# Kernel optimization log

Measured on AMD Instinct MI355X. Metric: run time of the kernel, lower is better.

## Reference

```python
import jax, jax.numpy as jnp
import numpy as np

BS, NA, NE, NAL = 128, 16, 16, 15
OWN, ALD, END = 30, 10, 10
H, HD, HYP, NACT = 64, 4, 64, 22
OUT_E = ((END + 1) * H + 1) * HD  # hyper_enemy output dim (weights + unused bias part)
OUT_A = ALD * H * HD


def setup_inputs() -> dict:
    key = jax.random.key(0)
    ks = jax.random.split(key, 30)
    s = 0.05
    r = lambda i, shape: jax.random.normal(ks[i], shape, dtype=jnp.float32) * s
    return {
        'bs': BS,
        'own_feats': r(0, (BS * NA, OWN)),
        'ally_feats': r(1, (BS * NA * NAL, ALD)),
        'enemy_feats': r(2, (BS * NA * NE, END)),
        'hidden_state': r(3, (BS * NA, H)),
        'fc1_w': r(4, (OWN, H)), 'fc1_b': r(5, (H,)),
        'he_w1': r(6, (END, HYP)), 'he_b1': r(7, (HYP,)),
        'he_w2': r(8, (HYP, OUT_E)), 'he_b2': r(9, (OUT_E,)),
        'ha_w1': r(10, (ALD, HYP)), 'ha_b1': r(11, (HYP,)),
        'ha_w2': r(12, (HYP, OUT_A)), 'ha_b2': r(13, (OUT_A,)),
        'merger_w': jnp.ones((1, HD, H), dtype=jnp.float32),
        'gru_wih': r(14, (3 * H, H)), 'gru_whh': r(15, (3 * H, H)),
        'gru_bih': r(16, (3 * H,)), 'gru_bhh': r(17, (3 * H,)),
        'fc2_w1': r(18, (H, H)), 'fc2_b1': r(19, (H,)),
        'fc2_w2': r(20, (H, NACT - 3)), 'fc2_b2': r(21, (NACT - 3,)),
        'pass_w1': r(22, (H, H)), 'pass_b1': r(23, (H,)),
        'pass_w2': r(24, (H, 3)), 'pass_b2': r(25, (3,)),
    }


def reference(bs, own_feats, ally_feats, enemy_feats, hidden_state,
              fc1_w, fc1_b, he_w1, he_b1, he_w2, he_b2,
              ha_w1, ha_b1, ha_w2, ha_b2, merger_w,
              gru_wih, gru_whh, gru_bih, gru_bhh,
              fc2_w1, fc2_b1, fc2_w2, fc2_b2,
              pass_w1, pass_b1, pass_w2, pass_b2):
    # own embedding: [bs*NA, H]
    emb_own = own_feats @ fc1_w + fc1_b

    # hypernet-generated enemy weights, consumed once then summed over enemies
    he = jax.nn.relu(enemy_feats @ he_w1 + he_b1) @ he_w2 + he_b2  # [bs*NA*NE, OUT_E]
    w_en = he[:, :END * H * HD].reshape(-1, END, H * HD)
    emb_en = jnp.einsum('ri,rio->ro', enemy_feats, w_en)
    emb_en = emb_en.reshape(bs * NA, NE, HD, H).sum(axis=1)  # [bs*NA, HD, H]

    ha = jax.nn.relu(ally_feats @ ha_w1 + ha_b1) @ ha_w2 + ha_b2  # [bs*NA*NAL, OUT_A]
    w_al = ha.reshape(-1, ALD, H * HD)
    emb_al4 = jnp.einsum('ri,rio->ro', ally_feats, w_al).reshape(bs * NA, NAL, HD, H)

    # passing_mlp -> [bs*NA, NAL, HD, 3]; permute/mean over heads, max over allies
    p = jax.nn.relu(emb_al4 @ pass_w1 + pass_b1) @ pass_w2 + pass_b2
    passing_dim = jnp.transpose(p, (0, 1, 3, 2)).mean(axis=-1)  # [bs*NA, NAL, 3]
    passing_embed = passing_dim.max(axis=1)  # [bs*NA, 3]

    emb_al = emb_al4.sum(axis=1)  # [bs*NA, HD, H]

    # Merger over heads
    mw = jax.nn.softmax(merger_w, axis=1)  # [1, HD, H]
    merged = jnp.sum(mw * (emb_en + emb_al), axis=1)  # [bs*NA, H]

    x = jax.nn.relu(emb_own + merged)

    # GRUCell (torch gate order: r, z, n)
    h_in = hidden_state.reshape(-1, H)
    gi = x @ gru_wih.T + gru_bih
    gh = h_in @ gru_whh.T + gru_bhh
    ir, iz, inn = jnp.split(gi, 3, axis=-1)
    hr, hz, hn = jnp.split(gh, 3, axis=-1)
    rg = jax.nn.sigmoid(ir + hr)
    zg = jax.nn.sigmoid(iz + hz)
    ng = jnp.tanh(inn + rg * hn)
    hh = (1.0 - zg) * ng + zg * h_in

    q_normal = (jax.nn.relu(hh @ fc2_w1 + fc2_b1) @ fc2_w2 + fc2_b2).reshape(bs, NA, -1)
    pe = passing_embed.reshape(bs, NA, 3)
    q = jnp.concatenate([q_normal[:, :, :9], pe, q_normal[:, :, 9:]], axis=-1)
    return q.reshape(bs, NA, -1), hh.reshape(bs, NA, -1)
```

## Files before the change

kernel.cpp:

```cpp
#include <hip/hip_runtime.h>
#include <hip/hip_bf16.h>

#define RAG   2048
#define AROWS 30720
#define KP    672
#define QOFF  45056

typedef __attribute__((ext_vector_type(8))) short short8;
typedef __attribute__((ext_vector_type(4))) float f32x4;

__device__ inline unsigned short f2bf(float f){
    unsigned u = __float_as_uint(f);
    u += 0x7fffu + ((u >> 16) & 1u);
    return (unsigned short)(u >> 16);
}
__device__ inline float bf2f(unsigned short s){ return __uint_as_float(((unsigned)s) << 16); }
__device__ inline unsigned pack2(float a, float b){
    return (unsigned)f2bf(a) | ((unsigned)f2bf(b) << 16);
}

__global__ void __launch_bounds__(256) k_prep(
    const float* __restrict__ hew2, const float* __restrict__ heb2,
    const float* __restrict__ haw2, const float* __restrict__ hab2,
    const float* __restrict__ allyf, const float* __restrict__ haw1, const float* __restrict__ hab1,
    unsigned short* __restrict__ Bte, unsigned short* __restrict__ Bta,
    unsigned short* __restrict__ ha1)
{
    int bb = blockIdx.x, tid = threadIdx.x;
    if (bb < 256){
        int n = bb;
        for (int k = tid; k < KP; k += 256){
            unsigned short ve = 0, va = 0;
            if (k < 640){
                int h = k & 63, i = k >> 6;
                ve = f2bf(hew2[h*2820 + i*256 + n]);
                va = f2bf(haw2[h*2560 + i*256 + n]);
            } else if (k < 650){
                int i = k - 640;
                ve = f2bf(heb2[i*256 + n]);
                va = f2bf(hab2[i*256 + n]);
            }
            Bte[n*KP + k] = ve;
            Bta[n*KP + k] = va;
        }
    } else {
        int r = (bb - 256)*4 + (tid >> 6), h = tid & 63;
        const float* a = allyf + r*10;
        float s = hab1[h];
#pragma unroll
        for (int i = 0; i < 10; ++i) s = fmaf(a[i], haw1[i*64 + h], s);
        ha1[r*64 + h] = f2bf(fmaxf(s, 0.f));
    }
}

__global__ void __launch_bounds__(256) k_usum(
    const float* __restrict__ ef, const float* __restrict__ hew1, const float* __restrict__ heb1,
    const float* __restrict__ af, const unsigned short* __restrict__ ha1,
    unsigned short* __restrict__ usum)
{
    __shared__ float s_ef[16][10], s_af[15][10];
    __shared__ float s_he[16][64], s_ha[15][64];
    int ag = blockIdx.x, tid = threadIdx.x;
    if (tid < 160) s_ef[tid/10][tid%10] = ef[ag*160 + tid];
    if (tid < 150) s_af[tid/10][tid%10] = af[ag*150 + tid];
    __syncthreads();
    for (int idx = tid; idx < 16*64; idx += 256){
        int en = idx >> 6, h = idx & 63;
        float s = heb1[h];
#pragma unroll
        for (int i = 0; i < 10; ++i) s = fmaf(s_ef[en][i], hew1[i*64 + h], s);
        s_he[en][h] = fmaxf(s, 0.f);
    }
    for (int idx = tid; idx < 15*64; idx += 256){
        int l = idx >> 6, h = idx & 63;
        s_ha[l][h] = bf2f(ha1[(ag*15 + l)*64 + h]);
    }
    __syncthreads();
    for (int k = tid; k < KP; k += 256){
        float ue = 0.f, ua = 0.f;
        if (k < 640){
            int i = k >> 6, h = k & 63;
#pragma unroll
            for (int en = 0; en < 16; ++en) ue = fmaf(s_he[en][h], s_ef[en][i], ue);
#pragma unroll
            for (int l = 0; l < 15; ++l) ua = fmaf(s_ha[l][h], s_af[l][i], ua);
        } else if (k < 650){
            int i = k - 640;
#pragma unroll
            for (int en = 0; en < 16; ++en) ue += s_ef[en][i];
#pragma unroll
            for (int l = 0; l < 15; ++l) ua += s_af[l][i];
        }
        usum[ag*KP + k]         = f2bf(ue);
        usum[(RAG + ag)*KP + k] = f2bf(ua);
    }
}

__global__ void __launch_bounds__(256, 2) k_gemm(
    const unsigned short* __restrict__ Bte, const unsigned short* __restrict__ Bta,
    const unsigned short* __restrict__ ha1, const float* __restrict__ af,
    const unsigned short* __restrict__ usum,
    const float* __restrict__ pw1, const float* __restrict__ pb1,
    const float* __restrict__ pw2, const float* __restrict__ pb2,
    float* __restrict__ emb, float* __restrict__ p2)
{
    __shared__ __align__(16) char smem[46080];
    unsigned short* sB  = (unsigned short*)smem;
    unsigned short* sA  = (unsigned short*)(smem + 20480);
    unsigned short* sH  = (unsigned short*)(smem + 25600);
    unsigned short* sW1 = (unsigned short*)(smem + 36864);

    int tid = threadIdx.x;
    int w = tid >> 6;
    int lane = tid & 63;
    int l15 = lane & 15, quad = lane >> 4;
    int bb = blockIdx.x;

    f32x4 acc[4][4];
#pragma unroll
    for (int a = 0; a < 4; ++a)
#pragma unroll
    for (int b = 0; b < 4; ++b) acc[a][b] = (f32x4){0.f, 0.f, 0.f, 0.f};

    if (bb < 480){
        int row0 = bb * 64;
        int r = tid >> 2, c = tid & 3;
#pragma unroll
        for (int p = 0; p < 2; ++p){
            int ch = tid + p*256;
            int rr = ch >> 3, cc = ch & 7;
            *(uint4*)&sH[rr*72 + cc*8] = *(const uint4*)&ha1[(row0 + rr)*64 + cc*8];
        }
#pragma unroll
        for (int p = 0; p < 16; ++p){
            int idx = tid + p*256;
            sW1[(idx & 63)*72 + (idx >> 6)] = f2bf(pw1[idx]);
        }
        float af_reg[10];
        {
            const float* ap = af + (row0 + r)*10;
#pragma unroll
            for (int i = 0; i < 10; ++i) af_reg[i] = ap[i];
        }
        __syncthreads();
        float h1f[16];
        {
            uint4 ra = *(const uint4*)&sH[r*72 + c*8];
            uint4 rb = *(const uint4*)&sH[r*72 + 32 + c*8];
            unsigned va[4] = {ra.x, ra.y, ra.z, ra.w};
            unsigned vb[4] = {rb.x, rb.y, rb.z, rb.w};
#pragma unroll
            for (int q = 0; q < 4; ++q){
                h1f[q*2+0]   = __uint_as_float(va[q] << 16);
                h1f[q*2+1]   = __uint_as_float(va[q] & 0xffff0000u);
                h1f[8+q*2+0] = __uint_as_float(vb[q] << 16);
                h1f[8+q*2+1] = __uint_as_float(vb[q] & 0xffff0000u);
            }
        }
        const unsigned short* Btb = Bta + tid*KP;
#pragma unroll
        for (int i = 0; i < 10; ++i){
#pragma unroll
            for (int hb = 0; hb < 2; ++hb){
                int kt = i*64 + hb*32;
                __syncthreads();
                uint4 bq0 = *(const uint4*)&Btb[kt + 0];
                uint4 bq1 = *(const uint4*)&Btb[kt + 8];
                uint4 bq2 = *(const uint4*)&Btb[kt + 16];
                uint4 bq3 = *(const uint4*)&Btb[kt + 24];
                float avf = af_reg[i];
                uint4 pk;
                pk.x = pack2(h1f[hb*8+0]*avf, h1f[hb*8+1]*avf);
                pk.y = pack2(h1f[hb*8+2]*avf, h1f[hb*8+3]*avf);
                pk.z = pack2(h1f[hb*8+4]*avf, h1f[hb*8+5]*avf);
                pk.w = pack2(h1f[hb*8+6]*avf, h1f[hb*8+7]*avf);
                *(uint4*)&sA[r*40 + c*8] = pk;
                *(uint4*)&sB[tid*40 + 0]  = bq0;
                *(uint4*)&sB[tid*40 + 8]  = bq1;
                *(uint4*)&sB[tid*40 + 16] = bq2;
                *(uint4*)&sB[tid*40 + 24] = bq3;
                __syncthreads();
                short8 a_[4], b_[4];
#pragma unroll
                for (int mt = 0; mt < 4; ++mt) a_[mt] = *(const short8*)&sA[(mt*16 + l15)*40 + quad*8];
#pragma unroll
                for (int nt = 0; nt < 4; ++nt) b_[nt] = *(const short8*)&sB[(w*64 + nt*16 + l15)*40 + quad*8];
#pragma unroll
                for (int mt = 0; mt < 4; ++mt)
#pragma unroll
                for (int nt = 0; nt < 4; ++nt)
                    acc[mt][nt] = __builtin_amdgcn_mfma_f32_16x16x32_bf16(a_[mt], b_[nt], acc[mt][nt], 0, 0, 0);
            }
        }
        {
            int kt = 640;
            __syncthreads();
            uint4 bq0 = *(const uint4*)&Btb[kt + 0];
            uint4 bq1 = *(const uint4*)&Btb[kt + 8];
            uint4 bq2 = *(const uint4*)&Btb[kt + 16];
            uint4 bq3 = *(const uint4*)&Btb[kt + 24];
            float v0=0.f,v1=0.f,v2=0.f,v3=0.f,v4=0.f,v5=0.f,v6=0.f,v7=0.f;
            if (c == 0){ v0=af_reg[0]; v1=af_reg[1]; v2=af_reg[2]; v3=af_reg[3];
                         v4=af_reg[4]; v5=af_reg[5]; v6=af_reg[6]; v7=af_reg[7]; }
            else if (c == 1){ v0 = af_reg[8]; v1 = af_reg[9]; }
            uint4 pk;
            pk.x = pack2(v0, v1); pk.y = pack2(v2, v3);
            pk.z = pack2(v4, v5); pk.w = pack2(v6, v7);
            *(uint4*)&sA[r*40 + c*8] = pk;
            *(uint4*)&sB[tid*40 + 0]  = bq0;
            *(uint4*)&sB[tid*40 + 8]  = bq1;
            *(uint4*)&sB[tid*40 + 16] = bq2;
            *(uint4*)&sB[tid*40 + 24] = bq3;
            __syncthreads();
            short8 a_[4], b_[4];
#pragma unroll
            for (int mt = 0; mt < 4; ++mt) a_[mt] = *(const short8*)&sA[(mt*16 + l15)*40 + quad*8];
#pragma unroll
            for (int nt = 0; nt < 4; ++nt) b_[nt] = *(const short8*)&sB[(w*64 + nt*16 + l15)*40 + quad*8];
#pragma unroll
            for (int mt = 0; mt < 4; ++mt)
#pragma unroll
            for (int nt = 0; nt < 4; ++nt)
                acc[mt][nt] = __builtin_amdgcn_mfma_f32_16x16x32_bf16(a_[mt], b_[nt], acc[mt][nt], 0, 0, 0);
        }
        __syncthreads();
        unsigned short* sE = (unsigned short*)(smem + w*9216);
#pragma unroll
        for (int mt = 0; mt < 4; ++mt)
#pragma unroll
        for (int nt = 0; nt < 4; ++nt)
#pragma unroll
        for (int rg = 0; rg < 4; ++rg)
            sE[(mt*16 + quad*4 + rg)*72 + nt*16 + l15] = f2bf(acc[mt][nt][rg]);
        __syncthreads();
        f32x4 yacc[4][4];
#pragma unroll
        for (int a = 0; a < 4; ++a)
#pragma unroll
        for (int b = 0; b < 4; ++b) yacc[a][b] = (f32x4){0.f, 0.f, 0.f, 0.f};
#pragma unroll
        for (int kb = 0; kb < 2; ++kb){
            short8 ea[4], wb[4];
#pragma unroll
            for (int mt = 0; mt < 4; ++mt) ea[mt] = *(const short8*)&sE[(mt*16 + l15)*72 + kb*32 + quad*8];
#pragma unroll
            for (int ot = 0; ot < 4; ++ot) wb[ot] = *(const short8*)&sW1[(ot*16 + l15)*72 + kb*32 + quad*8];
#pragma unroll
            for (int mt = 0; mt < 4; ++mt)
#pragma unroll
            for (int ot = 0; ot < 4; ++ot)
                yacc[mt][ot] = __builtin_amdgcn_mfma_f32_16x16x32_bf16(ea[mt], wb[ot], yacc[mt][ot], 0, 0, 0);
        }
        float pb1v[4], w2r[4][3];
#pragma unroll
        for (int ot = 0; ot < 4; ++ot){
            pb1v[ot] = pb1[ot*16 + l15];
#pragma unroll
            for (int j = 0; j < 3; ++j) w2r[ot][j] = pw2[(ot*16 + l15)*3 + j];
        }
#pragma unroll
        for (int mt = 0; mt < 4; ++mt){
            float part[4][3];
#pragma unroll
            for (int rg = 0; rg < 4; ++rg)
#pragma unroll
            for (int j = 0; j < 3; ++j) part[rg][j] = 0.f;
#pragma unroll
            for (int ot = 0; ot < 4; ++ot)
#pragma unroll
            for (int rg = 0; rg < 4; ++rg){
                float yv = fmaxf(yacc[mt][ot][rg] + pb1v[ot], 0.f);
#pragma unroll
                for (int j = 0; j < 3; ++j) part[rg][j] = fmaf(yv, w2r[ot][j], part[rg][j]);
            }
#pragma unroll
            for (int off = 1; off < 16; off <<= 1)
#pragma unroll
            for (int rg = 0; rg < 4; ++rg)
#pragma unroll
            for (int j = 0; j < 3; ++j) part[rg][j] += __shfl_xor(part[rg][j], off, 64);
            if (l15 == 0){
#pragma unroll
                for (int rg = 0; rg < 4; ++rg)
#pragma unroll
                for (int j = 0; j < 3; ++j)
                    p2[(row0 + mt*16 + quad*4 + rg)*12 + w*3 + j] = part[rg][j] + pb2[j];
            }
        }
    } else {
        int row0 = (bb - 480) * 64;
        const unsigned short* Btb = ((row0 < RAG) ? Bte : Bta) + tid*KP;
        const unsigned short* Ab  = usum + (row0 + (tid >> 2))*KP + (tid & 3)*8;
        int r = tid >> 2, c = tid & 3;
        for (int kt = 0; kt < KP; kt += 32){
            __syncthreads();
            uint4 aq  = *(const uint4*)&Ab[kt];
            uint4 bq0 = *(const uint4*)&Btb[kt + 0];
            uint4 bq1 = *(const uint4*)&Btb[kt + 8];
            uint4 bq2 = *(const uint4*)&Btb[kt + 16];
            uint4 bq3 = *(const uint4*)&Btb[kt + 24];
            *(uint4*)&sA[r*40 + c*8] = aq;
            *(uint4*)&sB[tid*40 + 0]  = bq0;
            *(uint4*)&sB[tid*40 + 8]  = bq1;
            *(uint4*)&sB[tid*40 + 16] = bq2;
            *(uint4*)&sB[tid*40 + 24] = bq3;
            __syncthreads();
            short8 a_[4], b_[4];
#pragma unroll
            for (int mt = 0; mt < 4; ++mt) a_[mt] = *(const short8*)&sA[(mt*16 + l15)*40 + quad*8];
#pragma unroll
            for (int nt = 0; nt < 4; ++nt) b_[nt] = *(const short8*)&sB[(w*64 + nt*16 + l15)*40 + quad*8];
#pragma unroll
            for (int mt = 0; mt < 4; ++mt)
#pragma unroll
            for (int nt = 0; nt < 4; ++nt)
                acc[mt][nt] = __builtin_amdgcn_mfma_f32_16x16x32_bf16(a_[mt], b_[nt], acc[mt][nt], 0, 0, 0);
        }
#pragma unroll
        for (int mt = 0; mt < 4; ++mt)
#pragma unroll
        for (int nt = 0; nt < 4; ++nt)
#pragma unroll
        for (int rg = 0; rg < 4; ++rg)
            emb[(row0 + mt*16 + quad*4 + rg)*256 + w*64 + nt*16 + l15] = acc[mt][nt][rg];
    }
}

__global__ void __launch_bounds__(512) k_final(
    const float* __restrict__ own, const float* __restrict__ hidden,
    const float* __restrict__ fc1w, const float* __restrict__ fc1b,
    const float* __restrict__ mergw,
    const float* __restrict__ wih, const float* __restrict__ whh,
    const float* __restrict__ bih, const float* __restrict__ bhh,
    const float* __restrict__ f2w1, const float* __restrict__ f2b1,
    const float* __restrict__ f2w2, const float* __restrict__ f2b2,
    const float* __restrict__ emb, const float* __restrict__ p2,
    float* __restrict__ out)
{
    int tid = threadIdx.x;
    int al = tid >> 6, h = tid & 63;
    int ag = blockIdx.x * 8 + al;
    __shared__ float sx[8][64], sh[8][64], sgi[8][192], sgh[8][192], shh[8][64], sq1[8][64];

    float s = fc1b[h];
    const float* ow = own + ag*30;
#pragma unroll
    for (int c = 0; c < 30; ++c) s = fmaf(ow[c], fc1w[c*64 + h], s);
    float m0 = mergw[h], m1 = mergw[64+h], m2 = mergw[128+h], m3 = mergw[192+h];
    float mx = fmaxf(fmaxf(m0, m1), fmaxf(m2, m3));
    float e0 = __expf(m0-mx), e1 = __expf(m1-mx), e2 = __expf(m2-mx), e3 = __expf(m3-mx);
    float inv = 1.f / (e0+e1+e2+e3);
    const float* een = emb + ag*256;
    const float* eal = emb + (RAG + ag)*256;
    float mg = (e0*(een[h]+eal[h]) + e1*(een[64+h]+eal[64+h]) +
                e2*(een[128+h]+eal[128+h]) + e3*(een[192+h]+eal[192+h])) * inv;
    sx[al][h] = fmaxf(s + mg, 0.f);
    sh[al][h] = hidden[ag*64 + h];
    __syncthreads();
    for (int g = h; g < 192; g += 64){
        float a = bih[g], b = bhh[g];
        for (int c0 = 0; c0 < 64; ++c0){
            a = fmaf(sx[al][c0], wih[g*64 + c0], a);
            b = fmaf(sh[al][c0], whh[g*64 + c0], b);
        }
        sgi[al][g] = a; sgh[al][g] = b;
    }
    __syncthreads();
    float rg = 1.f / (1.f + __expf(-(sgi[al][h] + sgh[al][h])));
    float zg = 1.f / (1.f + __expf(-(sgi[al][64+h] + sgh[al][64+h])));
    float ng = tanhf(sgi[al][128+h] + rg * sgh[al][128+h]);
    float hv = (1.f - zg)*ng + zg*sh[al][h];
    shh[al][h] = hv;
    __syncthreads();
    float q1 = f2b1[h];
    for (int c0 = 0; c0 < 64; ++c0) q1 = fmaf(shh[al][c0], f2w1[c0*64 + h], q1);
    sq1[al][h] = fmaxf(q1, 0.f);
    __syncthreads();
    float* qout = out + ag*22;
    if (h < 19){
        float s2 = f2b2[h];
        for (int c0 = 0; c0 < 64; ++c0) s2 = fmaf(sq1[al][c0], f2w2[c0*19 + h], s2);
        qout[(h < 9) ? h : h + 3] = s2;
    }
    if (h >= 32 && h < 35){
        int j = h - 32;
        float best = -1e30f;
        const float* pp = p2 + ag*15*12;
        for (int l = 0; l < 15; ++l){
            float mean = 0.25f*(pp[l*12+j] + pp[l*12+3+j] + pp[l*12+6+j] + pp[l*12+9+j]);
            best = fmaxf(best, mean);
        }
        qout[9 + j] = best;
    }
    out[QOFF + ag*64 + h] = hv;
}

extern "C" void kernel_launch(void* const* d_in, const int* in_sizes, int n_in,
                              void* d_out, int out_size, void* d_ws, size_t ws_size,
                              hipStream_t stream) {
    const float* own    = (const float*)d_in[1];
    const float* allyf  = (const float*)d_in[2];
    const float* enemyf = (const float*)d_in[3];
    const float* hidden = (const float*)d_in[4];
    const float* fc1w   = (const float*)d_in[5];
    const float* fc1b   = (const float*)d_in[6];
    const float* hew1   = (const float*)d_in[7];
    const float* heb1   = (const float*)d_in[8];
    const float* hew2   = (const float*)d_in[9];
    const float* heb2   = (const float*)d_in[10];
    const float* haw1   = (const float*)d_in[11];
    const float* hab1   = (const float*)d_in[12];
    const float* haw2   = (const float*)d_in[13];
    const float* hab2   = (const float*)d_in[14];
    const float* mergw  = (const float*)d_in[15];
    const float* wih    = (const float*)d_in[16];
    const float* whh    = (const float*)d_in[17];
    const float* bih    = (const float*)d_in[18];
    const float* bhh    = (const float*)d_in[19];
    const float* f2w1   = (const float*)d_in[20];
    const float* f2b1   = (const float*)d_in[21];
    const float* f2w2   = (const float*)d_in[22];
    const float* f2b2   = (const float*)d_in[23];
    const float* pw1    = (const float*)d_in[24];
    const float* pb1    = (const float*)d_in[25];
    const float* pw2    = (const float*)d_in[26];
    const float* pb2    = (const float*)d_in[27];
    float* out = (float*)d_out;

    char* W = (char*)d_ws;
    unsigned short* Bte  = (unsigned short*)(W + 0);
    unsigned short* Bta  = (unsigned short*)(W + 344064);
    unsigned short* ha1  = (unsigned short*)(W + 688128);
    unsigned short* usum = (unsigned short*)(W + 4620288);
    float*          emb  = (float*)(W + 10125312);
    float*          p2   = (float*)(W + 14319616);

    k_prep<<<256 + 7680, 256, 0, stream>>>(hew2, heb2, haw2, hab2, allyf, haw1, hab1, Bte, Bta, ha1);
    k_usum<<<RAG, 256, 0, stream>>>(enemyf, hew1, heb1, allyf, ha1, usum);
    k_gemm<<<480 + 64, 256, 0, stream>>>(Bte, Bta, ha1, allyf, usum, pw1, pb1, pw2, pb2, emb, p2);
    k_final<<<RAG/8, 512, 0, stream>>>(own, hidden, fc1w, fc1b, mergw, wih, whh, bih, bhh,
                                       f2w1, f2b1, f2w2, f2b2, emb, p2, out);
}
```

Before: 194.8 us.

## Fuse prep into usum, recompute ally hidden, MFMA GRU, rebalance gemm grid

Merges the weight-prep kernel into k_usum and drops the materialized ally hypernet hidden layer, recomputing it in k_usum and k_gemm from the raw ally features. That removes one launch and a large bf16 intermediate round trip through global memory. The final kernel now computes the GRU gate and fc2 first-layer matmuls with bf16 MFMA over 16 agents per block, using pre-packed bf16 weights, instead of scalar fp32 loops. The gemm grid is trimmed so each summed-embedding block handles two tiles. The costs are lower precision in the GRU path and more repeated arithmetic for the hidden-layer recompute.

```diff
diff --git a/kernel.cpp b/kernel.cpp
--- a/kernel.cpp
+++ b/kernel.cpp
@@ -2,7 +2,6 @@
 #include <hip/hip_bf16.h>
 
 #define RAG   2048
-#define AROWS 30720
 #define KP    672
 #define QOFF  45056
 
@@ -14,21 +13,23 @@
     u += 0x7fffu + ((u >> 16) & 1u);
     return (unsigned short)(u >> 16);
 }
-__device__ inline float bf2f(unsigned short s){ return __uint_as_float(((unsigned)s) << 16); }
 __device__ inline unsigned pack2(float a, float b){
     return (unsigned)f2bf(a) | ((unsigned)f2bf(b) << 16);
 }
 
-__global__ void __launch_bounds__(256) k_prep(
+__global__ void __launch_bounds__(256) k_usum(
+    const float* __restrict__ ef, const float* __restrict__ hew1, const float* __restrict__ heb1,
+    const float* __restrict__ af, const float* __restrict__ haw1, const float* __restrict__ hab1,
     const float* __restrict__ hew2, const float* __restrict__ heb2,
     const float* __restrict__ haw2, const float* __restrict__ hab2,
-    const float* __restrict__ allyf, const float* __restrict__ haw1, const float* __restrict__ hab1,
+    const float* __restrict__ wih, const float* __restrict__ whh, const float* __restrict__ f2w1,
     unsigned short* __restrict__ Bte, unsigned short* __restrict__ Bta,
-    unsigned short* __restrict__ ha1)
+    unsigned short* __restrict__ Wgru, unsigned short* __restrict__ B2,
+    unsigned short* __restrict__ usum)
 {
     int bb = blockIdx.x, tid = threadIdx.x;
-    if (bb < 256){
-        int n = bb;
+    if (bb >= RAG){
+        int n = bb - RAG;
         for (int k = tid; k < KP; k += 256){
             unsigned short ve = 0, va = 0;
             if (k < 640){
@@ -43,24 +44,19 @@
             Bte[n*KP + k] = ve;
             Bta[n*KP + k] = va;
         }
-    } else {
-        int r = (bb - 256)*4 + (tid >> 6), h = tid & 63;
-        const float* a = allyf + r*10;
-        float s = hab1[h];
-#pragma unroll
-        for (int i = 0; i < 10; ++i) s = fmaf(a[i], haw1[i*64 + h], s);
-        ha1[r*64 + h] = f2bf(fmaxf(s, 0.f));
-    }
-}
-
-__global__ void __launch_bounds__(256) k_usum(
-    const float* __restrict__ ef, const float* __restrict__ hew1, const float* __restrict__ heb1,
-    const float* __restrict__ af, const unsigned short* __restrict__ ha1,
-    unsigned short* __restrict__ usum)
-{
+        if (tid < 128){
+            int k = tid; float v;
+            if (n < 128)      v = (k < 64) ? wih[n*64 + k] : whh[n*64 + k - 64];
+            else if (n < 192) v = (k < 64) ? wih[n*64 + k] : 0.f;
+            else              v = (k < 64) ? 0.f : whh[(n-64)*64 + k - 64];
+            Wgru[n*128 + k] = f2bf(v);
+        }
+        if (n < 64 && tid < 64) B2[n*64 + tid] = f2bf(f2w1[tid*64 + n]);
+        return;
+    }
     __shared__ float s_ef[16][10], s_af[15][10];
     __shared__ float s_he[16][64], s_ha[15][64];
-    int ag = blockIdx.x, tid = threadIdx.x;
+    int ag = bb;
     if (tid < 160) s_ef[tid/10][tid%10] = ef[ag*160 + tid];
     if (tid < 150) s_af[tid/10][tid%10] = af[ag*150 + tid];
     __syncthreads();
@@ -73,7 +69,10 @@
     }
     for (int idx = tid; idx < 15*64; idx += 256){
         int l = idx >> 6, h = idx & 63;
-        s_ha[l][h] = bf2f(ha1[(ag*15 + l)*64 + h]);
+        float s = hab1[h];
+#pragma unroll
+        for (int i = 0; i < 10; ++i) s = fmaf(s_af[l][i], haw1[i*64 + h], s);
+        s_ha[l][h] = fmaxf(s, 0.f);
     }
     __syncthreads();
     for (int k = tid; k < KP; k += 256){
@@ -98,8 +97,8 @@
 
 __global__ void __launch_bounds__(256, 2) k_gemm(
     const unsigned short* __restrict__ Bte, const unsigned short* __restrict__ Bta,
-    const unsigned short* __restrict__ ha1, const float* __restrict__ af,
-    const unsigned short* __restrict__ usum,
+    const float* __restrict__ haw1, const float* __restrict__ hab1,
+    const float* __restrict__ af, const unsigned short* __restrict__ usum,
     const float* __restrict__ pw1, const float* __restrict__ pb1,
     const float* __restrict__ pw2, const float* __restrict__ pb2,
     float* __restrict__ emb, float* __restrict__ p2)
@@ -107,7 +106,6 @@
     __shared__ __align__(16) char smem[46080];
     unsigned short* sB  = (unsigned short*)smem;
     unsigned short* sA  = (unsigned short*)(smem + 20480);
-    unsigned short* sH  = (unsigned short*)(smem + 25600);
     unsigned short* sW1 = (unsigned short*)(smem + 36864);
 
     int tid = threadIdx.x;
@@ -116,21 +114,14 @@
     int l15 = lane & 15, quad = lane >> 4;
     int bb = blockIdx.x;
 
-    f32x4 acc[4][4];
-#pragma unroll
-    for (int a = 0; a < 4; ++a)
-#pragma unroll
-    for (int b = 0; b < 4; ++b) acc[a][b] = (f32x4){0.f, 0.f, 0.f, 0.f};
-
     if (bb < 480){
+        f32x4 acc[4][4];
+#pragma unroll
+        for (int a = 0; a < 4; ++a)
+#pragma unroll
+        for (int b = 0; b < 4; ++b) acc[a][b] = (f32x4){0.f, 0.f, 0.f, 0.f};
         int row0 = bb * 64;
         int r = tid >> 2, c = tid & 3;
-#pragma unroll
-        for (int p = 0; p < 2; ++p){
-            int ch = tid + p*256;
-            int rr = ch >> 3, cc = ch & 7;
-            *(uint4*)&sH[rr*72 + cc*8] = *(const uint4*)&ha1[(row0 + rr)*64 + cc*8];
-        }
 #pragma unroll
         for (int p = 0; p < 16; ++p){
             int idx = tid + p*256;
@@ -142,20 +133,18 @@
 #pragma unroll
             for (int i = 0; i < 10; ++i) af_reg[i] = ap[i];
         }
-        __syncthreads();
         float h1f[16];
-        {
-            uint4 ra = *(const uint4*)&sH[r*72 + c*8];
-            uint4 rb = *(const uint4*)&sH[r*72 + 32 + c*8];
-            unsigned va[4] = {ra.x, ra.y, ra.z, ra.w};
-            unsigned vb[4] = {rb.x, rb.y, rb.z, rb.w};
-#pragma unroll
-            for (int q = 0; q < 4; ++q){
-                h1f[q*2+0]   = __uint_as_float(va[q] << 16);
-                h1f[q*2+1]   = __uint_as_float(va[q] & 0xffff0000u);
-                h1f[8+q*2+0] = __uint_as_float(vb[q] << 16);
-                h1f[8+q*2+1] = __uint_as_float(vb[q] & 0xffff0000u);
-            }
+#pragma unroll
+        for (int q = 0; q < 8; ++q){
+            int h0 = c*8 + q, h1 = 32 + c*8 + q;
+            float v0 = hab1[h0], v1 = hab1[h1];
+#pragma unroll
+            for (int i = 0; i < 10; ++i){
+                v0 = fmaf(af_reg[i], haw1[i*64 + h0], v0);
+                v1 = fmaf(af_reg[i], haw1[i*64 + h1], v1);
+            }
+            h1f[q]     = fmaxf(v0, 0.f);
+            h1f[8 + q] = fmaxf(v1, 0.f);
         }
         const unsigned short* Btb = Bta + tid*KP;
 #pragma unroll
@@ -288,111 +277,178 @@
             }
         }
     } else {
-        int row0 = (bb - 480) * 64;
-        const unsigned short* Btb = ((row0 < RAG) ? Bte : Bta) + tid*KP;
-        const unsigned short* Ab  = usum + (row0 + (tid >> 2))*KP + (tid & 3)*8;
-        int r = tid >> 2, c = tid & 3;
-        for (int kt = 0; kt < KP; kt += 32){
-            __syncthreads();
-            uint4 aq  = *(const uint4*)&Ab[kt];
-            uint4 bq0 = *(const uint4*)&Btb[kt + 0];
-            uint4 bq1 = *(const uint4*)&Btb[kt + 8];
-            uint4 bq2 = *(const uint4*)&Btb[kt + 16];
-            uint4 bq3 = *(const uint4*)&Btb[kt + 24];
-            *(uint4*)&sA[r*40 + c*8] = aq;
-            *(uint4*)&sB[tid*40 + 0]  = bq0;
-            *(uint4*)&sB[tid*40 + 8]  = bq1;
-            *(uint4*)&sB[tid*40 + 16] = bq2;
-            *(uint4*)&sB[tid*40 + 24] = bq3;
-            __syncthreads();
-            short8 a_[4], b_[4];
-#pragma unroll
-            for (int mt = 0; mt < 4; ++mt) a_[mt] = *(const short8*)&sA[(mt*16 + l15)*40 + quad*8];
-#pragma unroll
-            for (int nt = 0; nt < 4; ++nt) b_[nt] = *(const short8*)&sB[(w*64 + nt*16 + l15)*40 + quad*8];
+        for (int rep = 0; rep < 2; ++rep){
+            int tile = (bb - 480)*2 + rep;
+            int row0 = tile * 64;
+            f32x4 acc[4][4];
+#pragma unroll
+            for (int a = 0; a < 4; ++a)
+#pragma unroll
+            for (int b = 0; b < 4; ++b) acc[a][b] = (f32x4){0.f, 0.f, 0.f, 0.f};
+            const unsigned short* Btb = ((row0 < RAG) ? Bte : Bta) + tid*KP;
+            const unsigned short* Ab  = usum + (row0 + (tid >> 2))*KP + (tid & 3)*8;
+            int r = tid >> 2, c = tid & 3;
+            for (int kt = 0; kt < KP; kt += 32){
+                __syncthreads();
+                uint4 aq  = *(const uint4*)&Ab[kt];
+                uint4 bq0 = *(const uint4*)&Btb[kt + 0];
+                uint4 bq1 = *(const uint4*)&Btb[kt + 8];
+                uint4 bq2 = *(const uint4*)&Btb[kt + 16];
+                uint4 bq3 = *(const uint4*)&Btb[kt + 24];
+                *(uint4*)&sA[r*40 + c*8] = aq;
+                *(uint4*)&sB[tid*40 + 0]  = bq0;
+                *(uint4*)&sB[tid*40 + 8]  = bq1;
+                *(uint4*)&sB[tid*40 + 16] = bq2;
+                *(uint4*)&sB[tid*40 + 24] = bq3;
+                __syncthreads();
+                short8 a_[4], b_[4];
+#pragma unroll
+                for (int mt = 0; mt < 4; ++mt) a_[mt] = *(const short8*)&sA[(mt*16 + l15)*40 + quad*8];
+#pragma unroll
+                for (int nt = 0; nt < 4; ++nt) b_[nt] = *(const short8*)&sB[(w*64 + nt*16 + l15)*40 + quad*8];
+#pragma unroll
+                for (int mt = 0; mt < 4; ++mt)
+#pragma unroll
+                for (int nt = 0; nt < 4; ++nt)
+                    acc[mt][nt] = __builtin_amdgcn_mfma_f32_16x16x32_bf16(a_[mt], b_[nt], acc[mt][nt], 0, 0, 0);
+            }
 #pragma unroll
             for (int mt = 0; mt < 4; ++mt)
 #pragma unroll
             for (int nt = 0; nt < 4; ++nt)
-                acc[mt][nt] = __builtin_amdgcn_mfma_f32_16x16x32_bf16(a_[mt], b_[nt], acc[mt][nt], 0, 0, 0);
-        }
-#pragma unroll
-        for (int mt = 0; mt < 4; ++mt)
-#pragma unroll
-        for (int nt = 0; nt < 4; ++nt)
-#pragma unroll
-        for (int rg = 0; rg < 4; ++rg)
-            emb[(row0 + mt*16 + quad*4 + rg)*256 + w*64 + nt*16 + l15] = acc[mt][nt][rg];
+#pragma unroll
+            for (int rg = 0; rg < 4; ++rg)
+                emb[(row0 + mt*16 + quad*4 + rg)*256 + w*64 + nt*16 + l15] = acc[mt][nt][rg];
+        }
     }
 }
 
-__global__ void __launch_bounds__(512) k_final(
+__global__ void __launch_bounds__(256) k_final(
     const float* __restrict__ own, const float* __restrict__ hidden,
     const float* __restrict__ fc1w, const float* __restrict__ fc1b,
     const float* __restrict__ mergw,
-    const float* __restrict__ wih, const float* __restrict__ whh,
     const float* __restrict__ bih, const float* __restrict__ bhh,
-    const float* __restrict__ f2w1, const float* __restrict__ f2b1,
-    const float* __restrict__ f2w2, const float* __restrict__ f2b2,
+    const float* __restrict__ f2b1, const float* __restrict__ f2w2, const float* __restrict__ f2b2,
+    const unsigned short* __restrict__ Wgru, const unsigned short* __restrict__ B2,
     const float* __restrict__ emb, const float* __restrict__ p2,
     float* __restrict__ out)
 {
+    __shared__ __align__(16) unsigned short sA16[16*128];
+    __shared__ float sHin[16*65];
+    __shared__ float sG[256*17];
+    __shared__ float sH2f[16*65];
+    __shared__ __align__(16) unsigned short sH2b[16*64];
+    __shared__ float sY[16*68];
+
     int tid = threadIdx.x;
-    int al = tid >> 6, h = tid & 63;
-    int ag = blockIdx.x * 8 + al;
-    __shared__ float sx[8][64], sh[8][64], sgi[8][192], sgh[8][192], shh[8][64], sq1[8][64];
-
-    float s = fc1b[h];
-    const float* ow = own + ag*30;
-#pragma unroll
-    for (int c = 0; c < 30; ++c) s = fmaf(ow[c], fc1w[c*64 + h], s);
-    float m0 = mergw[h], m1 = mergw[64+h], m2 = mergw[128+h], m3 = mergw[192+h];
-    float mx = fmaxf(fmaxf(m0, m1), fmaxf(m2, m3));
-    float e0 = __expf(m0-mx), e1 = __expf(m1-mx), e2 = __expf(m2-mx), e3 = __expf(m3-mx);
-    float inv = 1.f / (e0+e1+e2+e3);
-    const float* een = emb + ag*256;
-    const float* eal = emb + (RAG + ag)*256;
-    float mg = (e0*(een[h]+eal[h]) + e1*(een[64+h]+eal[64+h]) +
-                e2*(een[128+h]+eal[128+h]) + e3*(een[192+h]+eal[192+h])) * inv;
-    sx[al][h] = fmaxf(s + mg, 0.f);
-    sh[al][h] = hidden[ag*64 + h];
+    int w = tid >> 6, lane = tid & 63;
+    int l15 = lane & 15, quad = lane >> 4;
+    int ag0 = blockIdx.x * 16;
+
+#pragma unroll
+    for (int p = 0; p < 4; ++p){
+        int idx = tid + p*256;
+        int h = idx & 63, a = idx >> 6;
+        int ag = ag0 + a;
+        float s = fc1b[h];
+        const float* ow = own + ag*30;
+#pragma unroll
+        for (int c = 0; c < 30; ++c) s = fmaf(ow[c], fc1w[c*64 + h], s);
+        float m0 = mergw[h], m1 = mergw[64+h], m2 = mergw[128+h], m3 = mergw[192+h];
+        float mx = fmaxf(fmaxf(m0, m1), fmaxf(m2, m3));
+        float e0 = __expf(m0-mx), e1 = __expf(m1-mx), e2 = __expf(m2-mx), e3 = __expf(m3-mx);
+        float inv = 1.f / (e0+e1+e2+e3);
+        const float* een = emb + ag*256;
+        const float* eal = emb + (RAG + ag)*256;
+        float mg = (e0*(een[h]+eal[h]) + e1*(een[64+h]+eal[64+h]) +
+                    e2*(een[128+h]+eal[128+h]) + e3*(een[192+h]+eal[192+h])) * inv;
+        float x = fmaxf(s + mg, 0.f);
+        float hin = hidden[ag*64 + h];
+        sA16[a*128 + h]      = f2bf(x);
+        sA16[a*128 + 64 + h] = f2bf(hin);
+        sHin[a*65 + h] = hin;
+    }
     __syncthreads();
-    for (int g = h; g < 192; g += 64){
-        float a = bih[g], b = bhh[g];
-        for (int c0 = 0; c0 < 64; ++c0){
-            a = fmaf(sx[al][c0], wih[g*64 + c0], a);
-            b = fmaf(sh[al][c0], whh[g*64 + c0], b);
-        }
-        sgi[al][g] = a; sgh[al][g] = b;
+
+    {
+        f32x4 g_[4];
+#pragma unroll
+        for (int t = 0; t < 4; ++t) g_[t] = (f32x4){0.f,0.f,0.f,0.f};
+#pragma unroll
+        for (int ks = 0; ks < 4; ++ks){
+            int kt = ks*32;
+            short8 a8 = *(const short8*)&sA16[l15*128 + kt + quad*8];
+#pragma unroll
+            for (int t = 0; t < 4; ++t){
+                int col = (w*4 + t)*16 + l15;
+                short8 b8 = *(const short8*)&Wgru[col*128 + kt + quad*8];
+                g_[t] = __builtin_amdgcn_mfma_f32_16x16x32_bf16(a8, b8, g_[t], 0, 0, 0);
+            }
+        }
+#pragma unroll
+        for (int t = 0; t < 4; ++t){
+            int col = (w*4 + t)*16 + l15;
+#pragma unroll
+            for (int rg = 0; rg < 4; ++rg) sG[col*17 + quad*4 + rg] = g_[t][rg];
+        }
     }
     __syncthreads();
-    float rg = 1.f / (1.f + __expf(-(sgi[al][h] + sgh[al][h])));
-    float zg = 1.f / (1.f + __expf(-(sgi[al][64+h] + sgh[al][64+h])));
-    float ng = tanhf(sgi[al][128+h] + rg * sgh[al][128+h]);
-    float hv = (1.f - zg)*ng + zg*sh[al][h];
-    shh[al][h] = hv;
+
+#pragma unroll
+    for (int p = 0; p < 4; ++p){
+        int idx = tid + p*256;
+        int a = idx & 15, h = idx >> 4;
+        float rs  = sG[h*17 + a]        + bih[h]      + bhh[h];
+        float zs  = sG[(64+h)*17 + a]   + bih[64+h]   + bhh[64+h];
+        float in_ = sG[(128+h)*17 + a]  + bih[128+h];
+        float hn  = sG[(192+h)*17 + a]  + bhh[128+h];
+        float r = 1.f / (1.f + __expf(-rs));
+        float z = 1.f / (1.f + __expf(-zs));
+        float n = tanhf(in_ + r*hn);
+        float hv = (1.f - z)*n + z*sHin[a*65 + h];
+        sH2f[a*65 + h] = hv;
+        sH2b[a*64 + h] = f2bf(hv);
+    }
     __syncthreads();
-    float q1 = f2b1[h];
-    for (int c0 = 0; c0 < 64; ++c0) q1 = fmaf(shh[al][c0], f2w1[c0*64 + h], q1);
-    sq1[al][h] = fmaxf(q1, 0.f);
+
+    {
+        f32x4 y = (f32x4){0.f,0.f,0.f,0.f};
+#pragma unroll
+        for (int ks = 0; ks < 2; ++ks){
+            int kt = ks*32;
+            short8 a8 = *(const short8*)&sH2b[l15*64 + kt + quad*8];
+            short8 b8 = *(const short8*)&B2[(w*16 + l15)*64 + kt + quad*8];
+            y = __builtin_amdgcn_mfma_f32_16x16x32_bf16(a8, b8, y, 0, 0, 0);
+        }
+        float b1v = f2b1[w*16 + l15];
+#pragma unroll
+        for (int rg = 0; rg < 4; ++rg)
+            sY[(quad*4 + rg)*68 + w*16 + l15] = fmaxf(y[rg] + b1v, 0.f);
+    }
     __syncthreads();
-    float* qout = out + ag*22;
-    if (h < 19){
-        float s2 = f2b2[h];
-        for (int c0 = 0; c0 < 64; ++c0) s2 = fmaf(sq1[al][c0], f2w2[c0*19 + h], s2);
-        qout[(h < 9) ? h : h + 3] = s2;
-    }
-    if (h >= 32 && h < 35){
-        int j = h - 32;
+
+    for (int idx = tid; idx < 16*19; idx += 256){
+        int a = idx / 19, j = idx - a*19;
+        float s2 = f2b2[j];
+        for (int c = 0; c < 64; ++c) s2 = fmaf(sY[a*68 + c], f2w2[c*19 + j], s2);
+        out[(ag0 + a)*22 + ((j < 9) ? j : j + 3)] = s2;
+    }
+    if (tid < 48){
+        int a = tid / 3, j = tid - a*3;
         float best = -1e30f;
-        const float* pp = p2 + ag*15*12;
+        const float* pp = p2 + (ag0 + a)*180;
         for (int l = 0; l < 15; ++l){
-            float mean = 0.25f*(pp[l*12+j] + pp[l*12+3+j] + pp[l*12+6+j] + pp[l*12+9+j]);
+            float mean = 0.25f*(pp[l*12 + j] + pp[l*12 + 3 + j] + pp[l*12 + 6 + j] + pp[l*12 + 9 + j]);
             best = fmaxf(best, mean);
         }
-        qout[9 + j] = best;
-    }
-    out[QOFF + ag*64 + h] = hv;
+        out[(ag0 + a)*22 + 9 + j] = best;
+    }
+#pragma unroll
+    for (int p = 0; p < 4; ++p){
+        int idx = tid + p*256;
+        int h = idx & 63, a = idx >> 6;
+        out[QOFF + (ag0 + a)*64 + h] = sH2f[a*65 + h];
+    }
 }
 
 extern "C" void kernel_launch(void* const* d_in, const int* in_sizes, int n_in,
@@ -430,14 +486,18 @@
     char* W = (char*)d_ws;
     unsigned short* Bte  = (unsigned short*)(W + 0);
     unsigned short* Bta  = (unsigned short*)(W + 344064);
-    unsigned short* ha1  = (unsigned short*)(W + 688128);
-    unsigned short* usum = (unsigned short*)(W + 4620288);
-    float*          emb  = (float*)(W + 10125312);
-    float*          p2   = (float*)(W + 14319616);
-
-    k_prep<<<256 + 7680, 256, 0, stream>>>(hew2, heb2, haw2, hab2, allyf, haw1, hab1, Bte, Bta, ha1);
-    k_usum<<<RAG, 256, 0, stream>>>(enemyf, hew1, heb1, allyf, ha1, usum);
-    k_gemm<<<480 + 64, 256, 0, stream>>>(Bte, Bta, ha1, allyf, usum, pw1, pb1, pw2, pb2, emb, p2);
-    k_final<<<RAG/8, 512, 0, stream>>>(own, hidden, fc1w, fc1b, mergw, wih, whh, bih, bhh,
-                                       f2w1, f2b1, f2w2, f2b2, emb, p2, out);
+    unsigned short* usum = (unsigned short*)(W + 688128);
+    float*          emb  = (float*)(W + 6193152);
+    float*          p2   = (float*)(W + 10387456);
+    unsigned short* Wgru = (unsigned short*)(W + 11862016);
+    unsigned short* B2   = (unsigned short*)(W + 11927552);
+
+    k_usum<<<RAG + 256, 256, 0, stream>>>(enemyf, hew1, heb1, allyf, haw1, hab1,
+                                          hew2, heb2, haw2, hab2, wih, whh, f2w1,
+                                          Bte, Bta, Wgru, B2, usum);
+    k_gemm<<<512, 256, 0, stream>>>(Bte, Bta, haw1, hab1, allyf, usum,
+                                    pw1, pb1, pw2, pb2, emb, p2);
+    k_final<<<RAG/16, 256, 0, stream>>>(own, hidden, fc1w, fc1b, mergw,
+                                        bih, bhh, f2b1, f2w2, f2b2,
+                                        Wgru, B2, emb, p2, out);
 }
```

After: 201.8 us. 3.6% more time.
